# Performance work log

Hardware: AMD Instinct MI355X
Metric: run time of the kernel (lower is better)

Reference implementation:

```python
import jax, jax.numpy as jnp
import numpy as np

H = 256
NUM_CONVS = 4
NUM_GRAPHS = 1024
N_PER_GRAPH = 32
ORDER = 3
NUM_TYPES = 22  # len(utils.BOND_TYPES)
NUM_NOISE_LEVEL = 50
ANNEAL_POWER = 2.0


def _build_graph():
    # Chain molecules extended to order-3 neighbors (mimics extend_graph on a path graph):
    # for |i-j| in [1,ORDER]: edge_order=|i-j|, edge_type = bond type if order 1 else NUM_TYPES+order-1.
    n = N_PER_GRAPH
    i, j = np.meshgrid(np.arange(n), np.arange(n), indexing='ij')
    dist = np.abs(i - j)
    mask = (dist >= 1) & (dist <= ORDER)
    src_l, dst_l, eo = i[mask], j[mask], dist[mask]
    offs = np.arange(NUM_GRAPHS)[:, None] * n
    src = (src_l[None, :] + offs).reshape(-1)
    dst = (dst_l[None, :] + offs).reshape(-1)
    edge_order = np.tile(eo, NUM_GRAPHS)
    rng = np.random.default_rng(0)
    bond_t = rng.integers(1, 5, size=edge_order.shape)
    edge_type = np.where(edge_order == 1, bond_t, NUM_TYPES + edge_order - 1)
    node2graph = np.repeat(np.arange(NUM_GRAPHS), n)
    return src, dst, edge_type, node2graph


def setup_inputs() -> dict:
    key = jax.random.key(0)
    ks = jax.random.split(key, 24)
    src, dst, edge_type, node2graph = _build_graph()
    N, E = node2graph.shape[0], src.shape[0]
    w = lambda k, s: (jax.random.normal(k, s, jnp.float32) * 0.05)
    sigmas = jnp.asarray(np.exp(np.linspace(np.log(10.0), np.log(0.01), NUM_NOISE_LEVEL)), dtype=jnp.float32)
    return {
        'atom_type': jnp.asarray(np.random.default_rng(1).integers(0, 100, N), jnp.int32),
        'edge_index': jnp.asarray(np.stack([src, dst]), jnp.int32),
        'edge_type': jnp.asarray(edge_type, jnp.int32),
        'node2graph': jnp.asarray(node2graph, jnp.int32),
        'noise_level': jax.random.randint(ks[0], (NUM_GRAPHS,), 0, NUM_NOISE_LEVEL, jnp.int32),
        'pos': jax.random.normal(ks[1], (N, 3), jnp.float32) * 3.0,
        'd_noise': jax.random.normal(ks[2], (E, 1), jnp.float32),
        'sigmas': sigmas,
        'node_emb': w(ks[3], (100, H)), 'edge_emb': w(ks[4], (100, H)),
        'in_W1': w(ks[5], (1, H)), 'in_b1': w(ks[6], (H,)),
        'in_W2': w(ks[7], (H, H)), 'in_b2': w(ks[8], (H,)),
        'gin_W1': w(ks[9], (NUM_CONVS, H, H)), 'gin_b1': w(ks[10], (NUM_CONVS, H)),
        'gin_W2': w(ks[11], (NUM_CONVS, H, H)), 'gin_b2': w(ks[12], (NUM_CONVS, H)),
        'out_W1': w(ks[13], (2 * H, H)), 'out_b1': w(ks[14], (H,)),
        'out_W2': w(ks[15], (H, H // 2)), 'out_b2': w(ks[16], (H // 2,)),
        'out_W3': w(ks[17], (H // 2, 1)), 'out_b3': w(ks[18], (1,)),
    }


def reference(atom_type, edge_index, edge_type, node2graph, noise_level,
              pos, d_noise, sigmas, node_emb, edge_emb,
              in_W1, in_b1, in_W2, in_b2,
              gin_W1, gin_b1, gin_W2, gin_b2,
              out_W1, out_b1, out_W2, out_b2, out_W3, out_b3):
    N = pos.shape[0]
    G = noise_level.shape[0]
    row, col = edge_index[0], edge_index[1]
    edge2graph = node2graph[row]                                  # [E]
    d = jnp.linalg.norm(pos[row] - pos[col], axis=-1, keepdims=True)  # [E,1]
    used_sigmas = sigmas[noise_level][edge2graph][:, None]        # [E,1]
    perturbed_d = d + d_noise * used_sigmas
    target = -(perturbed_d - d) / used_sigmas ** 2
    # embeddings + input MLP (Linear-relu-Linear)
    node_attr = node_emb[atom_type]                               # [N,H]
    d_emb = jax.nn.relu(perturbed_d @ in_W1 + in_b1) @ in_W2 + in_b2
    edge_attr = d_emb * edge_emb[edge_type]                       # [E,H]
    # GIN with GINE convs: agg = sum_j relu(x_j + e_ij); out = MLP(x + agg); relu between convs; residual
    x = node_attr
    n_convs = gin_W1.shape[0]
    for k in range(n_convs):
        msg = jax.nn.relu(x[row] + edge_attr)                     # [E,H]
        agg = jax.ops.segment_sum(msg, col, num_segments=N)       # [N,H]
        h = jax.nn.relu((x + agg) @ gin_W1[k] + gin_b1[k]) @ gin_W2[k] + gin_b2[k]
        if k < n_convs - 1:
            h = jax.nn.relu(h)
        x = h + x  # short_cut
    # edge score head
    feat = jnp.concatenate([x[row] * x[col], edge_attr], axis=-1)  # [E,2H]
    s = jax.nn.relu(feat @ out_W1 + out_b1)
    s = jax.nn.relu(s @ out_W2 + out_b2)
    s = s @ out_W3 + out_b3                                       # [E,1]
    scores = (s / used_sigmas).reshape(-1)
    t = target.reshape(-1)
    loss_e = 0.5 * (scores - t) ** 2 * used_sigmas.reshape(-1) ** ANNEAL_POWER
    return jax.ops.segment_sum(loss_e, edge2graph, num_segments=G)  # [G]
```

## Files before the change

kernel.cpp:

```cpp
#include <hip/hip_runtime.h>
#include <math.h>

typedef unsigned int u32;
typedef __attribute__((ext_vector_type(8))) short bf16x8;
typedef __attribute__((ext_vector_type(4))) float f32x4;

#define MFMA16(a,b,c) __builtin_amdgcn_mfma_f32_16x16x32_bf16(a,b,c,0,0,0)

__device__ inline u32 bf16r(float x){
  u32 u = __float_as_uint(x);
  return (u + 0x7fffu + ((u >> 16) & 1u)) >> 16;
}
__device__ inline u32 pack2(float a, float b){ return bf16r(a) | (bf16r(b) << 16); }
__device__ inline uint4 pack8(const float* f){
  uint4 v; v.x = pack2(f[0],f[1]); v.y = pack2(f[2],f[3]);
  v.z = pack2(f[4],f[5]); v.w = pack2(f[6],f[7]); return v;
}
__device__ inline float bf2f(short s){ return __uint_as_float(((u32)(unsigned short)s) << 16); }

__device__ __forceinline__ void gload_lds16(const void* g, void* l){
  __builtin_amdgcn_global_load_lds((const __attribute__((address_space(1))) unsigned int*)g,
                                   (__attribute__((address_space(3))) unsigned int*)l,
                                   16, 0, 0);
}

__device__ __forceinline__ int frag_off(int f, int quad){
  return (f>>1)*64 + (f&1)*32 + ((quad ^ ((f>>1)&3))*8);
}

__device__ __forceinline__ int xg2(int g, int r){ return g ^ ((r ^ (g>>1)) & 7); }

__global__ void k_cvtAll(const float* __restrict__ inW2, const float* __restrict__ gW1,
                         const float* __restrict__ gW2, const float* __restrict__ oW1,
                         const float* __restrict__ oW2,
                         short* __restrict__ w2t, short* __restrict__ gw1t,
                         short* __restrict__ gw2t, short* __restrict__ ow1t,
                         short* __restrict__ ow2t){
  int gidx = blockIdx.x*256 + threadIdx.x;
  const float* src; short* dst; int t, K8, Nf;
  if (gidx < 8192)      { src = inW2; dst = w2t; t = gidx; K8 = 32; Nf = 256; }
  else if (gidx < 40960){ int r = gidx-8192;  int c = r>>13; t = r&8191;
                          src = gW1 + (size_t)c*65536; dst = gw1t + (size_t)c*65536; K8 = 32; Nf = 256; }
  else if (gidx < 73728){ int r = gidx-40960; int c = r>>13; t = r&8191;
                          src = gW2 + (size_t)c*65536; dst = gw2t + (size_t)c*65536; K8 = 32; Nf = 256; }
  else if (gidx < 90112){ t = gidx-73728; src = oW1; dst = ow1t; K8 = 64; Nf = 256; }
  else if (gidx < 94208){ t = gidx-90112; src = oW2; dst = ow2t; K8 = 32; Nf = 128; }
  else return;
  int f = t / K8, c = t - f*K8;
  float v[8];
  #pragma unroll
  for (int j=0;j<8;j++) v[j] = src[(size_t)(c*8+j)*Nf + f];
  ((uint4*)dst)[t] = pack8(v);
}

__global__ void k_pre(const int* __restrict__ ei, const int* __restrict__ n2g,
                      const int* __restrict__ nl, const float* __restrict__ sigmas,
                      const float* __restrict__ pos, const float* __restrict__ dn, int E,
                      float* __restrict__ pd, int* __restrict__ cnt, int* __restrict__ inlist){
  int e = blockIdx.x*256 + threadIdx.x;
  if (e >= E) return;
  int r = ei[e], c = ei[E+e];
  float sg = sigmas[nl[n2g[r]]];
  float dx = pos[3*r]-pos[3*c], dy = pos[3*r+1]-pos[3*c+1], dz = pos[3*r+2]-pos[3*c+2];
  float d = sqrtf(dx*dx + dy*dy + dz*dz);
  pd[e] = d + dn[e]*sg;
  int slot = atomicAdd(&cnt[c], 1);
  if (slot < 8) inlist[c*8 + slot] = e;
}

__global__ __launch_bounds__(256) void k_attr(
    const float* __restrict__ pd, const float* __restrict__ W1, const float* __restrict__ b1,
    const short* __restrict__ W2t, const float* __restrict__ b2,
    const int* __restrict__ etype, const float* __restrict__ eemb,
    short* __restrict__ attr, int E)
{
  int tid = threadIdx.x;
  int base = blockIdx.x*64;
  int wv = tid>>6, lane = tid&63, quad = lane>>4, l15 = lane&15;
  float pdv[4];
  #pragma unroll
  for (int nt=0;nt<4;nt++) pdv[nt] = pd[base + nt*16 + l15];
  f32x4 acc[4][4];
  #pragma unroll
  for (int mt=0;mt<4;mt++) for (int nt=0;nt<4;nt++) acc[mt][nt] = (f32x4)0.f;
  #pragma unroll
  for (int s=0; s<8; s++){
    int k0 = s*32 + quad*8;
    float4 w1a = *(const float4*)(W1 + k0), w1b = *(const float4*)(W1 + k0 + 4);
    float4 b1a = *(const float4*)(b1 + k0), b1b = *(const float4*)(b1 + k0 + 4);
    bf16x8 a[4], b[4];
    #pragma unroll
    for (int mt=0;mt<4;mt++){
      int f = (wv*4+mt)*16 + l15;
      a[mt] = *(const bf16x8*)(W2t + (size_t)f*256 + k0);
    }
    #pragma unroll
    for (int nt=0;nt<4;nt++){
      float p = pdv[nt];
      float f[8] = {fmaxf(p*w1a.x+b1a.x,0.f), fmaxf(p*w1a.y+b1a.y,0.f),
                    fmaxf(p*w1a.z+b1a.z,0.f), fmaxf(p*w1a.w+b1a.w,0.f),
                    fmaxf(p*w1b.x+b1b.x,0.f), fmaxf(p*w1b.y+b1b.y,0.f),
                    fmaxf(p*w1b.z+b1b.z,0.f), fmaxf(p*w1b.w+b1b.w,0.f)};
      uint4 u = pack8(f);
      b[nt] = *(bf16x8*)&u;
    }
    #pragma unroll
    for (int mt=0;mt<4;mt++)
      #pragma unroll
      for (int nt=0;nt<4;nt++)
        acc[mt][nt] = MFMA16(a[mt], b[nt], acc[mt][nt]);
  }
  #pragma unroll
  for (int nt=0;nt<4;nt++){
    int e = base + nt*16 + l15;
    int et = etype[e];
    #pragma unroll
    for (int mt=0;mt<4;mt++){
      int f0 = (wv*4+mt)*16 + quad*4;
      float4 bb = *(const float4*)(b2 + f0);
      float4 em = *(const float4*)(eemb + (size_t)et*256 + f0);
      float v0 = (acc[mt][nt][0]+bb.x)*em.x, v1 = (acc[mt][nt][1]+bb.y)*em.y;
      float v2 = (acc[mt][nt][2]+bb.z)*em.z, v3 = (acc[mt][nt][3]+bb.w)*em.w;
      uint2 v; v.x = pack2(v0,v1); v.y = pack2(v2,v3);
      *(uint2*)(attr + (size_t)e*256 + f0) = v;
    }
  }
}

__global__ __launch_bounds__(512,4) void k_conv4(
    const int* __restrict__ at, const float* __restrict__ nemb,
    const short* __restrict__ attrS, const int* __restrict__ ei,
    const int* __restrict__ cnt, const int* __restrict__ inlist,
    const short* __restrict__ gw1t, const float* __restrict__ gb1,
    const short* __restrict__ gw2t, const float* __restrict__ gb2,
    short* __restrict__ xF, int E)
{
  __shared__ short xls[33*256];
  __shared__ uint4 AlsV[32*32];
  short* Als = (short*)AlsV;
  short* T1  = (short*)AlsV;
  int tid = threadIdx.x;
  int nbase = blockIdx.x*32;
  int wv = tid>>6, lane = tid&63, quad = lane>>4, l15 = lane&15;
  int jl = tid>>4, ch = tid&15;

  int topo[8];
  {
    int j = nbase + jl;
    int deg = min(cnt[j], 8);
    int4 L0 = *(const int4*)(inlist + j*8);
    int4 L1 = *(const int4*)(inlist + j*8 + 4);
    int raw[8] = {L0.x,L0.y,L0.z,L0.w,L1.x,L1.y,L1.z,L1.w};
    #pragma unroll
    for (int s=0;s<8;s++){
      int e = (s < deg) ? raw[s] : E;
      int r = ei[e] - nbase;
      if (s >= deg) r = 32;
      topo[s] = e | (r << 20);
    }
  }
  {
    int a = at[nbase + jl];
    const float* src = nemb + (size_t)a*256 + ch*16;
    float f[16];
    #pragma unroll
    for (int q=0;q<4;q++){
      float4 v = *(const float4*)(src + q*4);
      f[q*4]=v.x; f[q*4+1]=v.y; f[q*4+2]=v.z; f[q*4+3]=v.w;
    }
    *(uint4*)(xls + jl*256 + xg2(ch*2,   jl)*8) = pack8(f);
    *(uint4*)(xls + jl*256 + xg2(ch*2+1, jl)*8) = pack8(f+8);
    if (tid < 32){ uint4 z; z.x=z.y=z.z=z.w=0u; ((uint4*)(xls + 32*256))[tid] = z; }
  }
  __syncthreads();
  for (int c=0; c<4; c++){
    const short* W1t = gw1t + (size_t)c*65536;
    const short* W2t = gw2t + (size_t)c*65536;
    const float* b1 = gb1 + c*256;
    const float* b2 = gb2 + c*256;
    #pragma unroll
    for (int qq=0; qq<2; qq++){
      int cc = ch*2 + qq;
      float f[8];
      {
        bf16x8 v0 = *(const bf16x8*)(xls + jl*256 + xg2(cc, jl)*8);
        #pragma unroll
        for (int j=0;j<8;j++) f[j]=bf2f(v0[j]);
      }
      #pragma unroll
      for (int s=0; s<8; s++){
        int e = topo[s] & 0xFFFFF;
        int r = topo[s] >> 20;
        bf16x8 x0 = *(const bf16x8*)(xls + r*256 + xg2(cc, r)*8);
        bf16x8 a0 = *(const bf16x8*)(attrS + (size_t)e*256 + ch*16 + qq*8);
        #pragma unroll
        for (int j=0;j<8;j++) f[j] += fmaxf(bf2f(x0[j]) + bf2f(a0[j]), 0.f);
      }
      *(uint4*)(Als + jl*256 + ((cc ^ (jl&7))*8)) = pack8(f);
    }
    __syncthreads();
    f32x4 acc[2][2];
    #pragma unroll
    for (int mt=0;mt<2;mt++) for (int nt=0;nt<2;nt++) acc[mt][nt] = (f32x4)0.f;
    #pragma unroll
    for (int s=0; s<8; s++){
      bf16x8 a[2], b[2];
      #pragma unroll
      for (int mt=0;mt<2;mt++)
        a[mt] = *(const bf16x8*)(W1t + (size_t)((wv*2+mt)*16 + l15)*256 + s*32 + quad*8);
      #pragma unroll
      for (int nt=0;nt<2;nt++){
        int n = nt*16 + l15; int cc = s*4 + quad;
        b[nt] = *(const bf16x8*)(Als + n*256 + ((cc ^ (n&7))*8));
      }
      #pragma unroll
      for (int mt=0;mt<2;mt++)
        #pragma unroll
        for (int nt=0;nt<2;nt++)
          acc[mt][nt] = MFMA16(a[mt], b[nt], acc[mt][nt]);
    }
    __syncthreads();
    #pragma unroll
    for (int mt=0;mt<2;mt++){
      int f0 = (wv*2+mt)*16 + quad*4;
      float4 bb = *(const float4*)(b1 + f0);
      int cg = f0 >> 3, off = (quad&1)*4;
      #pragma unroll
      for (int nt=0;nt<2;nt++){
        int n = nt*16 + l15;
        float v0 = fmaxf(acc[mt][nt][0]+bb.x,0.f), v1 = fmaxf(acc[mt][nt][1]+bb.y,0.f);
        float v2 = fmaxf(acc[mt][nt][2]+bb.z,0.f), v3 = fmaxf(acc[mt][nt][3]+bb.w,0.f);
        uint2 v; v.x = pack2(v0,v1); v.y = pack2(v2,v3);
        *(uint2*)(T1 + n*256 + ((cg ^ (n&7))*8) + off) = v;
      }
    }
    __syncthreads();
    f32x4 acc2[2][2];
    #pragma unroll
    for (int mt=0;mt<2;mt++) for (int nt=0;nt<2;nt++) acc2[mt][nt] = (f32x4)0.f;
    #pragma unroll
    for (int s=0; s<8; s++){
      bf16x8 a[2], b[2];
      #pragma unroll
      for (int mt=0;mt<2;mt++)
        a[mt] = *(const bf16x8*)(W2t + (size_t)((wv*2+mt)*16 + l15)*256 + s*32 + quad*8);
      #pragma unroll
      for (int nt=0;nt<2;nt++){
        int n = nt*16 + l15; int cc = s*4 + quad;
        b[nt] = *(const bf16x8*)(T1 + n*256 + ((cc ^ (n&7))*8));
      }
      #pragma unroll
      for (int mt=0;mt<2;mt++)
        #pragma unroll
        for (int nt=0;nt<2;nt++)
          acc2[mt][nt] = MFMA16(a[mt], b[nt], acc2[mt][nt]);
    }
    #pragma unroll
    for (int mt=0;mt<2;mt++){
      int f0 = (wv*2+mt)*16 + quad*4;
      float4 bb = *(const float4*)(b2 + f0);
      int g2 = f0 >> 3, half = (quad&1)*4;
      #pragma unroll
      for (int nt=0;nt<2;nt++){
        int n = nt*16 + l15;
        short* px = xls + n*256 + xg2(g2, n)*8 + half;
        uint2 old = *(uint2*)px;
        float o0 = __uint_as_float(old.x<<16), o1 = __uint_as_float(old.x&0xffff0000u);
        float o2 = __uint_as_float(old.y<<16), o3 = __uint_as_float(old.y&0xffff0000u);
        float h0 = acc2[mt][nt][0]+bb.x, h1 = acc2[mt][nt][1]+bb.y;
        float h2 = acc2[mt][nt][2]+bb.z, h3 = acc2[mt][nt][3]+bb.w;
        if (c < 3){ h0=fmaxf(h0,0.f); h1=fmaxf(h1,0.f); h2=fmaxf(h2,0.f); h3=fmaxf(h3,0.f); }
        uint2 v; v.x = pack2(o0+h0, o1+h1); v.y = pack2(o2+h2, o3+h3);
        *(uint2*)px = v;
      }
    }
    __syncthreads();
  }
  {
    uint4 v0 = *(const uint4*)(xls + jl*256 + xg2(ch*2,   jl)*8);
    uint4 v1 = *(const uint4*)(xls + jl*256 + xg2(ch*2+1, jl)*8);
    *(uint4*)(xF + (size_t)(nbase+jl)*256 + ch*16)     = v0;
    *(uint4*)(xF + (size_t)(nbase+jl)*256 + ch*16 + 8) = v1;
  }
}

__global__ __launch_bounds__(512,2) void k_head(
    const short* __restrict__ xF, const short* __restrict__ attrS,
    const int* __restrict__ ei,
    const short* __restrict__ W1t, const float* __restrict__ ob1,
    const short* __restrict__ W2t, const float* __restrict__ ob2,
    const float* __restrict__ W3, const float* __restrict__ ob3,
    const float* __restrict__ dnoise, const int* __restrict__ n2g,
    float* __restrict__ out, int E, int G)
{
  __shared__ uint4 BlsV[16*256];
  __shared__ float Sedge[64];
  __shared__ float part[4];
  short* Bls = (short*)BlsV;
  short* T   = (short*)BlsV;
  int tid = threadIdx.x;
  int base = blockIdx.x*64;
  int wv = tid>>6, lane = tid&63, quad = lane>>4, l15 = lane&15;
  if (tid < 64) Sedge[tid] = 0.f;
  if (tid < 4) part[tid] = 0.f;
  int g8 = tid & 255, sh = tid >> 8, w4 = g8 >> 6;
  {
    int p = g8>>3, hi = (g8>>2)&1, cs = g8&3;
    int n = p*2 + hi, cc = cs ^ (p&3);
    const short* srcb = attrS + (size_t)(base+n)*256 + cc*8;
    #pragma unroll
    for (int i=0;i<4;i++){
      int s = 8 + i*2 + sh;
      gload_lds16(srcb + (s-8)*32, (char*)BlsV + (size_t)s*4096 + w4*1024);
    }
  }
  {
    int p = g8>>3, hi = (g8>>2)&1, cs = g8&3;
    int n = p*2 + hi, cc = cs ^ (p&3);
    int rr = ei[base+n], rc = ei[E+base+n];
    const short* xr = xF + (size_t)rr*256 + cc*8;
    const short* xc = xF + (size_t)rc*256 + cc*8;
    #pragma unroll
    for (int i=0;i<4;i++){
      int s = sh*4 + i;
      bf16x8 va = *(const bf16x8*)(xr + s*32);
      bf16x8 vb = *(const bf16x8*)(xc + s*32);
      float f[8];
      #pragma unroll
      for (int j=0;j<8;j++) f[j] = bf2f(va[j])*bf2f(vb[j]);
      *(uint4*)(Bls + (size_t)s*2048 + g8*8) = pack8(f);
    }
  }
  __syncthreads();
  f32x4 acc[2][4];
  #pragma unroll
  for (int mt=0;mt<2;mt++) for (int nt=0;nt<4;nt++) acc[mt][nt] = (f32x4)0.f;
  #pragma unroll
  for (int s=0; s<16; s++){
    bf16x8 a[2], b[4];
    #pragma unroll
    for (int mt=0;mt<2;mt++)
      a[mt] = *(const bf16x8*)(W1t + (size_t)((wv*2+mt)*16 + l15)*512 + s*32 + quad*8);
    #pragma unroll
    for (int nt=0;nt<4;nt++)
      b[nt] = *(const bf16x8*)(Bls + (size_t)s*2048 + frag_off(nt*16 + l15, quad));
    #pragma unroll
    for (int mt=0;mt<2;mt++)
      #pragma unroll
      for (int nt=0;nt<4;nt++)
        acc[mt][nt] = MFMA16(a[mt], b[nt], acc[mt][nt]);
  }
  __syncthreads();
  #pragma unroll
  for (int mt=0;mt<2;mt++){
    int f0 = (wv*2+mt)*16 + quad*4;
    float4 bb = *(const float4*)(ob1 + f0);
    int c = f0 >> 3, off = (quad&1)*4;
    #pragma unroll
    for (int nt=0;nt<4;nt++){
      int n = nt*16 + l15;
      float v0 = fmaxf(acc[mt][nt][0]+bb.x,0.f), v1 = fmaxf(acc[mt][nt][1]+bb.y,0.f);
      float v2 = fmaxf(acc[mt][nt][2]+bb.z,0.f), v3 = fmaxf(acc[mt][nt][3]+bb.w,0.f);
      uint2 v; v.x = pack2(v0,v1); v.y = pack2(v2,v3);
      *(uint2*)(T + n*256 + ((c ^ (n&7))*8) + off) = v;
    }
  }
  __syncthreads();
  f32x4 acc2[4];
  #pragma unroll
  for (int nt=0;nt<4;nt++) acc2[nt] = (f32x4)0.f;
  #pragma unroll
  for (int s=0; s<8; s++){
    bf16x8 a = *(const bf16x8*)(W2t + (size_t)(wv*16 + l15)*256 + s*32 + quad*8);
    #pragma unroll
    for (int nt=0;nt<4;nt++){
      int n = nt*16 + l15; int cc = s*4 + quad;
      bf16x8 b = *(const bf16x8*)(T + n*256 + ((cc ^ (n&7))*8));
      acc2[nt] = MFMA16(a, b, acc2[nt]);
    }
  }
  {
    int f0 = wv*16 + quad*4;
    float4 bb = *(const float4*)(ob2 + f0);
    float4 w3 = *(const float4*)(W3 + f0);
    #pragma unroll
    for (int nt=0;nt<4;nt++){
      float p = fmaxf(acc2[nt][0]+bb.x,0.f)*w3.x + fmaxf(acc2[nt][1]+bb.y,0.f)*w3.y
              + fmaxf(acc2[nt][2]+bb.z,0.f)*w3.z + fmaxf(acc2[nt][3]+bb.w,0.f)*w3.w;
      p += __shfl_xor(p, 16);
      p += __shfl_xor(p, 32);
      if (lane < 16) atomicAdd(&Sedge[nt*16 + l15], p);
    }
  }
  __syncthreads();
  int gbase = n2g[ei[base]];
  if (tid < 64){
    int e = base + tid;
    float sv = Sedge[tid] + ob3[0] + dnoise[e];
    float l = 0.5f*sv*sv;
    int g = n2g[ei[e]] - gbase;
    atomicAdd(&part[g & 3], l);
  }
  __syncthreads();
  if (tid < 2 && (gbase + tid) < G)
    atomicAdd(&out[gbase + tid], part[tid]);
}

static inline size_t alignup(size_t v){ return (v + 255) & ~(size_t)255; }

extern "C" void kernel_launch(void* const* d_in, const int* in_sizes, int n_in,
                              void* d_out, int out_size, void* d_ws, size_t ws_size,
                              hipStream_t stream) {
  const int*   at    = (const int*)  d_in[0];
  const int*   ei    = (const int*)  d_in[1];
  const int*   etype = (const int*)  d_in[2];
  const int*   n2g   = (const int*)  d_in[3];
  const int*   nl    = (const int*)  d_in[4];
  const float* pos   = (const float*)d_in[5];
  const float* dnoi  = (const float*)d_in[6];
  const float* sig   = (const float*)d_in[7];
  const float* nemb  = (const float*)d_in[8];
  const float* eemb  = (const float*)d_in[9];
  const float* inW1  = (const float*)d_in[10];
  const float* inb1  = (const float*)d_in[11];
  const float* inW2  = (const float*)d_in[12];
  const float* inb2  = (const float*)d_in[13];
  const float* gW1   = (const float*)d_in[14];
  const float* gb1   = (const float*)d_in[15];
  const float* gW2   = (const float*)d_in[16];
  const float* gb2   = (const float*)d_in[17];
  const float* oW1   = (const float*)d_in[18];
  const float* ob1   = (const float*)d_in[19];
  const float* oW2   = (const float*)d_in[20];
  const float* ob2   = (const float*)d_in[21];
  const float* oW3   = (const float*)d_in[22];
  const float* ob3   = (const float*)d_in[23];
  float* out = (float*)d_out;

  const int N = in_sizes[0];
  const int E = in_sizes[2];
  const int G = in_sizes[4];
  const int H = 256;

  char* w = (char*)d_ws;
  size_t off = 0;
  size_t o_attr  = off; off = alignup(off + (size_t)(E+1)*H*2);
  size_t o_xF    = off; off = alignup(off + (size_t)N*H*2);
  size_t o_pd    = off; off = alignup(off + (size_t)E*4);
  size_t o_cnt   = off; off = alignup(off + (size_t)N*4);
  size_t o_inl   = off; off = alignup(off + (size_t)N*8*4);
  size_t o_w2t   = off; off = alignup(off + (size_t)H*H*2);
  size_t o_gw1t  = off; off = alignup(off + (size_t)4*H*H*2);
  size_t o_gw2t  = off; off = alignup(off + (size_t)4*H*H*2);
  size_t o_ow1t  = off; off = alignup(off + (size_t)H*2*H*2);
  size_t o_ow2t  = off; off = alignup(off + (size_t)(H/2)*H*2);
  (void)ws_size; (void)n_in; (void)out_size;

  short* attrS = (short*)(w + o_attr);
  short* xF    = (short*)(w + o_xF);
  float* pd    = (float*)(w + o_pd);
  int*   cnt   = (int*)  (w + o_cnt);
  int*   inl   = (int*)  (w + o_inl);
  short* w2t   = (short*)(w + o_w2t);
  short* gw1t  = (short*)(w + o_gw1t);
  short* gw2t  = (short*)(w + o_gw2t);
  short* ow1t  = (short*)(w + o_ow1t);
  short* ow2t  = (short*)(w + o_ow2t);

  hipMemsetAsync(cnt, 0, (size_t)N*4, stream);
  hipMemsetAsync(out, 0, (size_t)G*4, stream);
  hipMemsetAsync(attrS + (size_t)E*H, 0, (size_t)H*2, stream);

  k_cvtAll<<<368, 256, 0, stream>>>(inW2, gW1, gW2, oW1, oW2,
                                    w2t, gw1t, gw2t, ow1t, ow2t);

  k_pre<<<(E+255)/256, 256, 0, stream>>>(ei, n2g, nl, sig, pos, dnoi, E, pd, cnt, inl);
  k_attr<<<E/64, 256, 0, stream>>>(pd, inW1, inb1, w2t, inb2, etype, eemb, attrS, E);

  k_conv4<<<G, 512, 0, stream>>>(at, nemb, attrS, ei, cnt, inl,
                                 gw1t, gb1, gw2t, gb2, xF, E);

  k_head<<<E/64, 512, 0, stream>>>(xF, attrS, ei, ow1t, ob1, ow2t, ob2,
                                   oW3, ob3, dnoi, n2g, out, E, G);
}
```

Before: 555.7 us.

## Switch storage and MFMA from bf16 to fp16 with packed half arithmetic

Converts all weights, activations and edge attributes from bf16 to fp16, using cvt_pkrtz for packing and f16 MFMA instead of bf16 MFMA. The message aggregation, residual add and edge-product elementwise work now run as packed half2 add/relu/mul rather than unpacking to fp32 and repacking with software rounding. It also gives the conv kernel a separate T1 LDS buffer so one barrier can be removed, and lowers the occupancy hint to 3 blocks. Accumulating the aggregation sums in fp16 risks overflow or precision loss, and the extra LDS may reduce occupancy.

```diff
diff --git a/kernel.cpp b/kernel.cpp
--- a/kernel.cpp
+++ b/kernel.cpp
@@ -2,21 +2,31 @@
 #include <math.h>
 
 typedef unsigned int u32;
-typedef __attribute__((ext_vector_type(8))) short bf16x8;
+typedef __attribute__((ext_vector_type(2))) _Float16 h2;
+typedef __attribute__((ext_vector_type(8))) _Float16 h8;
 typedef __attribute__((ext_vector_type(4))) float f32x4;
 
-#define MFMA16(a,b,c) __builtin_amdgcn_mfma_f32_16x16x32_bf16(a,b,c,0,0,0)
-
-__device__ inline u32 bf16r(float x){
-  u32 u = __float_as_uint(x);
-  return (u + 0x7fffu + ((u >> 16) & 1u)) >> 16;
-}
-__device__ inline u32 pack2(float a, float b){ return bf16r(a) | (bf16r(b) << 16); }
-__device__ inline uint4 pack8(const float* f){
-  uint4 v; v.x = pack2(f[0],f[1]); v.y = pack2(f[2],f[3]);
-  v.z = pack2(f[4],f[5]); v.w = pack2(f[6],f[7]); return v;
-}
-__device__ inline float bf2f(short s){ return __uint_as_float(((u32)(unsigned short)s) << 16); }
+#define MFMA16H(a,b,c) __builtin_amdgcn_mfma_f32_16x16x32_f16(a,b,c,0,0,0)
+
+__device__ __forceinline__ u32 pkrtz(float a, float b){
+  auto r = __builtin_amdgcn_cvt_pkrtz(a, b);
+  return *(u32*)&r;
+}
+__device__ __forceinline__ uint4 pack8h(const float* f){
+  uint4 v; v.x = pkrtz(f[0],f[1]); v.y = pkrtz(f[2],f[3]);
+  v.z = pkrtz(f[4],f[5]); v.w = pkrtz(f[6],f[7]); return v;
+}
+__device__ __forceinline__ u32 pk_add(u32 a, u32 b){
+  h2 r = *(h2*)&a + *(h2*)&b; return *(u32*)&r;
+}
+__device__ __forceinline__ u32 pk_mul(u32 a, u32 b){
+  h2 r = *(h2*)&a * *(h2*)&b; return *(u32*)&r;
+}
+__device__ __forceinline__ u32 pk_relu(u32 a){
+  h2 z = {(_Float16)0.f, (_Float16)0.f};
+  h2 r = __builtin_elementwise_max(*(h2*)&a, z);
+  return *(u32*)&r;
+}
 
 __device__ __forceinline__ void gload_lds16(const void* g, void* l){
   __builtin_amdgcn_global_load_lds((const __attribute__((address_space(1))) unsigned int*)g,
@@ -50,7 +60,7 @@
   float v[8];
   #pragma unroll
   for (int j=0;j<8;j++) v[j] = src[(size_t)(c*8+j)*Nf + f];
-  ((uint4*)dst)[t] = pack8(v);
+  ((uint4*)dst)[t] = pack8h(v);
 }
 
 __global__ void k_pre(const int* __restrict__ ei, const int* __restrict__ n2g,
@@ -88,11 +98,11 @@
     int k0 = s*32 + quad*8;
     float4 w1a = *(const float4*)(W1 + k0), w1b = *(const float4*)(W1 + k0 + 4);
     float4 b1a = *(const float4*)(b1 + k0), b1b = *(const float4*)(b1 + k0 + 4);
-    bf16x8 a[4], b[4];
+    h8 a[4], b[4];
     #pragma unroll
     for (int mt=0;mt<4;mt++){
       int f = (wv*4+mt)*16 + l15;
-      a[mt] = *(const bf16x8*)(W2t + (size_t)f*256 + k0);
+      a[mt] = *(const h8*)(W2t + (size_t)f*256 + k0);
     }
     #pragma unroll
     for (int nt=0;nt<4;nt++){
@@ -101,14 +111,14 @@
                     fmaxf(p*w1a.z+b1a.z,0.f), fmaxf(p*w1a.w+b1a.w,0.f),
                     fmaxf(p*w1b.x+b1b.x,0.f), fmaxf(p*w1b.y+b1b.y,0.f),
                     fmaxf(p*w1b.z+b1b.z,0.f), fmaxf(p*w1b.w+b1b.w,0.f)};
-      uint4 u = pack8(f);
-      b[nt] = *(bf16x8*)&u;
+      uint4 u = pack8h(f);
+      b[nt] = *(h8*)&u;
     }
     #pragma unroll
     for (int mt=0;mt<4;mt++)
       #pragma unroll
       for (int nt=0;nt<4;nt++)
-        acc[mt][nt] = MFMA16(a[mt], b[nt], acc[mt][nt]);
+        acc[mt][nt] = MFMA16H(a[mt], b[nt], acc[mt][nt]);
   }
   #pragma unroll
   for (int nt=0;nt<4;nt++){
@@ -121,13 +131,13 @@
       float4 em = *(const float4*)(eemb + (size_t)et*256 + f0);
       float v0 = (acc[mt][nt][0]+bb.x)*em.x, v1 = (acc[mt][nt][1]+bb.y)*em.y;
       float v2 = (acc[mt][nt][2]+bb.z)*em.z, v3 = (acc[mt][nt][3]+bb.w)*em.w;
-      uint2 v; v.x = pack2(v0,v1); v.y = pack2(v2,v3);
+      uint2 v; v.x = pkrtz(v0,v1); v.y = pkrtz(v2,v3);
       *(uint2*)(attr + (size_t)e*256 + f0) = v;
     }
   }
 }
 
-__global__ __launch_bounds__(512,4) void k_conv4(
+__global__ __launch_bounds__(512,3) void k_conv4(
     const int* __restrict__ at, const float* __restrict__ nemb,
     const short* __restrict__ attrS, const int* __restrict__ ei,
     const int* __restrict__ cnt, const int* __restrict__ inlist,
@@ -137,8 +147,9 @@
 {
   __shared__ short xls[33*256];
   __shared__ uint4 AlsV[32*32];
+  __shared__ uint4 T1V [32*32];
   short* Als = (short*)AlsV;
-  short* T1  = (short*)AlsV;
+  short* T1  = (short*)T1V;
   int tid = threadIdx.x;
   int nbase = blockIdx.x*32;
   int wv = tid>>6, lane = tid&63, quad = lane>>4, l15 = lane&15;
@@ -168,8 +179,8 @@
       float4 v = *(const float4*)(src + q*4);
       f[q*4]=v.x; f[q*4+1]=v.y; f[q*4+2]=v.z; f[q*4+3]=v.w;
     }
-    *(uint4*)(xls + jl*256 + xg2(ch*2,   jl)*8) = pack8(f);
-    *(uint4*)(xls + jl*256 + xg2(ch*2+1, jl)*8) = pack8(f+8);
+    *(uint4*)(xls + jl*256 + xg2(ch*2,   jl)*8) = pack8h(f);
+    *(uint4*)(xls + jl*256 + xg2(ch*2+1, jl)*8) = pack8h(f+8);
     if (tid < 32){ uint4 z; z.x=z.y=z.z=z.w=0u; ((uint4*)(xls + 32*256))[tid] = z; }
   }
   __syncthreads();
@@ -178,25 +189,29 @@
     const short* W2t = gw2t + (size_t)c*65536;
     const float* b1 = gb1 + c*256;
     const float* b2 = gb2 + c*256;
-    #pragma unroll
-    for (int qq=0; qq<2; qq++){
-      int cc = ch*2 + qq;
-      float f[8];
-      {
-        bf16x8 v0 = *(const bf16x8*)(xls + jl*256 + xg2(cc, jl)*8);
-        #pragma unroll
-        for (int j=0;j<8;j++) f[j]=bf2f(v0[j]);
-      }
+    {
+      uint4 A0 = *(const uint4*)(xls + jl*256 + xg2(ch*2,   jl)*8);
+      uint4 A1 = *(const uint4*)(xls + jl*256 + xg2(ch*2+1, jl)*8);
       #pragma unroll
       for (int s=0; s<8; s++){
         int e = topo[s] & 0xFFFFF;
         int r = topo[s] >> 20;
-        bf16x8 x0 = *(const bf16x8*)(xls + r*256 + xg2(cc, r)*8);
-        bf16x8 a0 = *(const bf16x8*)(attrS + (size_t)e*256 + ch*16 + qq*8);
-        #pragma unroll
-        for (int j=0;j<8;j++) f[j] += fmaxf(bf2f(x0[j]) + bf2f(a0[j]), 0.f);
+        uint4 x0 = *(const uint4*)(xls + r*256 + xg2(ch*2,   r)*8);
+        uint4 x1 = *(const uint4*)(xls + r*256 + xg2(ch*2+1, r)*8);
+        const short* ar = attrS + (size_t)e*256 + ch*16;
+        uint4 a0 = *(const uint4*)(ar);
+        uint4 a1 = *(const uint4*)(ar + 8);
+        A0.x = pk_add(A0.x, pk_relu(pk_add(x0.x, a0.x)));
+        A0.y = pk_add(A0.y, pk_relu(pk_add(x0.y, a0.y)));
+        A0.z = pk_add(A0.z, pk_relu(pk_add(x0.z, a0.z)));
+        A0.w = pk_add(A0.w, pk_relu(pk_add(x0.w, a0.w)));
+        A1.x = pk_add(A1.x, pk_relu(pk_add(x1.x, a1.x)));
+        A1.y = pk_add(A1.y, pk_relu(pk_add(x1.y, a1.y)));
+        A1.z = pk_add(A1.z, pk_relu(pk_add(x1.z, a1.z)));
+        A1.w = pk_add(A1.w, pk_relu(pk_add(x1.w, a1.w)));
       }
-      *(uint4*)(Als + jl*256 + ((cc ^ (jl&7))*8)) = pack8(f);
+      *(uint4*)(Als + jl*256 + (((ch*2  ) ^ (jl&7))*8)) = A0;
+      *(uint4*)(Als + jl*256 + (((ch*2+1) ^ (jl&7))*8)) = A1;
     }
     __syncthreads();
     f32x4 acc[2][2];
@@ -204,22 +219,21 @@
     for (int mt=0;mt<2;mt++) for (int nt=0;nt<2;nt++) acc[mt][nt] = (f32x4)0.f;
     #pragma unroll
     for (int s=0; s<8; s++){
-      bf16x8 a[2], b[2];
+      h8 a[2], b[2];
       #pragma unroll
       for (int mt=0;mt<2;mt++)
-        a[mt] = *(const bf16x8*)(W1t + (size_t)((wv*2+mt)*16 + l15)*256 + s*32 + quad*8);
+        a[mt] = *(const h8*)(W1t + (size_t)((wv*2+mt)*16 + l15)*256 + s*32 + quad*8);
       #pragma unroll
       for (int nt=0;nt<2;nt++){
         int n = nt*16 + l15; int cc = s*4 + quad;
-        b[nt] = *(const bf16x8*)(Als + n*256 + ((cc ^ (n&7))*8));
+        b[nt] = *(const h8*)(Als + n*256 + ((cc ^ (n&7))*8));
       }
       #pragma unroll
       for (int mt=0;mt<2;mt++)
         #pragma unroll
         for (int nt=0;nt<2;nt++)
-          acc[mt][nt] = MFMA16(a[mt], b[nt], acc[mt][nt]);
-    }
-    __syncthreads();
+          acc[mt][nt] = MFMA16H(a[mt], b[nt], acc[mt][nt]);
+    }
     #pragma unroll
     for (int mt=0;mt<2;mt++){
       int f0 = (wv*2+mt)*16 + quad*4;
@@ -230,7 +244,7 @@
         int n = nt*16 + l15;
         float v0 = fmaxf(acc[mt][nt][0]+bb.x,0.f), v1 = fmaxf(acc[mt][nt][1]+bb.y,0.f);
         float v2 = fmaxf(acc[mt][nt][2]+bb.z,0.f), v3 = fmaxf(acc[mt][nt][3]+bb.w,0.f);
-        uint2 v; v.x = pack2(v0,v1); v.y = pack2(v2,v3);
+        uint2 v; v.x = pkrtz(v0,v1); v.y = pkrtz(v2,v3);
         *(uint2*)(T1 + n*256 + ((cg ^ (n&7))*8) + off) = v;
       }
     }
@@ -240,20 +254,20 @@
     for (int mt=0;mt<2;mt++) for (int nt=0;nt<2;nt++) acc2[mt][nt] = (f32x4)0.f;
     #pragma unroll
     for (int s=0; s<8; s++){
-      bf16x8 a[2], b[2];
+      h8 a[2], b[2];
       #pragma unroll
       for (int mt=0;mt<2;mt++)
-        a[mt] = *(const bf16x8*)(W2t + (size_t)((wv*2+mt)*16 + l15)*256 + s*32 + quad*8);
+        a[mt] = *(const h8*)(W2t + (size_t)((wv*2+mt)*16 + l15)*256 + s*32 + quad*8);
       #pragma unroll
       for (int nt=0;nt<2;nt++){
         int n = nt*16 + l15; int cc = s*4 + quad;
-        b[nt] = *(const bf16x8*)(T1 + n*256 + ((cc ^ (n&7))*8));
+        b[nt] = *(const h8*)(T1 + n*256 + ((cc ^ (n&7))*8));
       }
       #pragma unroll
       for (int mt=0;mt<2;mt++)
         #pragma unroll
         for (int nt=0;nt<2;nt++)
-          acc2[mt][nt] = MFMA16(a[mt], b[nt], acc2[mt][nt]);
+          acc2[mt][nt] = MFMA16H(a[mt], b[nt], acc2[mt][nt]);
     }
     #pragma unroll
     for (int mt=0;mt<2;mt++){
@@ -265,12 +279,10 @@
         int n = nt*16 + l15;
         short* px = xls + n*256 + xg2(g2, n)*8 + half;
         uint2 old = *(uint2*)px;
-        float o0 = __uint_as_float(old.x<<16), o1 = __uint_as_float(old.x&0xffff0000u);
-        float o2 = __uint_as_float(old.y<<16), o3 = __uint_as_float(old.y&0xffff0000u);
-        float h0 = acc2[mt][nt][0]+bb.x, h1 = acc2[mt][nt][1]+bb.y;
-        float h2 = acc2[mt][nt][2]+bb.z, h3 = acc2[mt][nt][3]+bb.w;
-        if (c < 3){ h0=fmaxf(h0,0.f); h1=fmaxf(h1,0.f); h2=fmaxf(h2,0.f); h3=fmaxf(h3,0.f); }
-        uint2 v; v.x = pack2(o0+h0, o1+h1); v.y = pack2(o2+h2, o3+h3);
+        u32 n0 = pkrtz(acc2[mt][nt][0]+bb.x, acc2[mt][nt][1]+bb.y);
+        u32 n1 = pkrtz(acc2[mt][nt][2]+bb.z, acc2[mt][nt][3]+bb.w);
+        if (c < 3){ n0 = pk_relu(n0); n1 = pk_relu(n1); }
+        uint2 v; v.x = pk_add(old.x, n0); v.y = pk_add(old.y, n1);
         *(uint2*)px = v;
       }
     }
@@ -323,12 +335,11 @@
     #pragma unroll
     for (int i=0;i<4;i++){
       int s = sh*4 + i;
-      bf16x8 va = *(const bf16x8*)(xr + s*32);
-      bf16x8 vb = *(const bf16x8*)(xc + s*32);
-      float f[8];
-      #pragma unroll
-      for (int j=0;j<8;j++) f[j] = bf2f(va[j])*bf2f(vb[j]);
-      *(uint4*)(Bls + (size_t)s*2048 + g8*8) = pack8(f);
+      uint4 va = *(const uint4*)(xr + s*32);
+      uint4 vb = *(const uint4*)(xc + s*32);
+      uint4 pr; pr.x = pk_mul(va.x, vb.x); pr.y = pk_mul(va.y, vb.y);
+      pr.z = pk_mul(va.z, vb.z); pr.w = pk_mul(va.w, vb.w);
+      *(uint4*)(Bls + (size_t)s*2048 + g8*8) = pr;
     }
   }
   __syncthreads();
@@ -337,18 +348,18 @@
   for (int mt=0;mt<2;mt++) for (int nt=0;nt<4;nt++) acc[mt][nt] = (f32x4)0.f;
   #pragma unroll
   for (int s=0; s<16; s++){
-    bf16x8 a[2], b[4];
+    h8 a[2], b[4];
     #pragma unroll
     for (int mt=0;mt<2;mt++)
-      a[mt] = *(const bf16x8*)(W1t + (size_t)((wv*2+mt)*16 + l15)*512 + s*32 + quad*8);
+      a[mt] = *(const h8*)(W1t + (size_t)((wv*2+mt)*16 + l15)*512 + s*32 + quad*8);
     #pragma unroll
     for (int nt=0;nt<4;nt++)
-      b[nt] = *(const bf16x8*)(Bls + (size_t)s*2048 + frag_off(nt*16 + l15, quad));
+      b[nt] = *(const h8*)(Bls + (size_t)s*2048 + frag_off(nt*16 + l15, quad));
     #pragma unroll
     for (int mt=0;mt<2;mt++)
       #pragma unroll
       for (int nt=0;nt<4;nt++)
-        acc[mt][nt] = MFMA16(a[mt], b[nt], acc[mt][nt]);
+        acc[mt][nt] = MFMA16H(a[mt], b[nt], acc[mt][nt]);
   }
   __syncthreads();
   #pragma unroll
@@ -361,7 +372,7 @@
       int n = nt*16 + l15;
       float v0 = fmaxf(acc[mt][nt][0]+bb.x,0.f), v1 = fmaxf(acc[mt][nt][1]+bb.y,0.f);
       float v2 = fmaxf(acc[mt][nt][2]+bb.z,0.f), v3 = fmaxf(acc[mt][nt][3]+bb.w,0.f);
-      uint2 v; v.x = pack2(v0,v1); v.y = pack2(v2,v3);
+      uint2 v; v.x = pkrtz(v0,v1); v.y = pkrtz(v2,v3);
       *(uint2*)(T + n*256 + ((c ^ (n&7))*8) + off) = v;
     }
   }
@@ -371,12 +382,12 @@
   for (int nt=0;nt<4;nt++) acc2[nt] = (f32x4)0.f;
   #pragma unroll
   for (int s=0; s<8; s++){
-    bf16x8 a = *(const bf16x8*)(W2t + (size_t)(wv*16 + l15)*256 + s*32 + quad*8);
+    h8 a = *(const h8*)(W2t + (size_t)(wv*16 + l15)*256 + s*32 + quad*8);
     #pragma unroll
     for (int nt=0;nt<4;nt++){
       int n = nt*16 + l15; int cc = s*4 + quad;
-      bf16x8 b = *(const bf16x8*)(T + n*256 + ((cc ^ (n&7))*8));
-      acc2[nt] = MFMA16(a, b, acc2[nt]);
+      h8 b = *(const h8*)(T + n*256 + ((cc ^ (n&7))*8));
+      acc2[nt] = MFMA16H(a, b, acc2[nt]);
     }
   }
   {
```

New measurement: 540.4 us. -2.8%, faster.
